# Optimization experiments

Measured on AMD Instinct MI355X. Metric: run time of the kernel, lower is better.

## Reference

```python
import jax, jax.numpy as jnp
import numpy as np

N_VERTS, N_RADIAL, N_ANGULAR, FEAT = 100000, 5, 8, 16
AMT_TEMPLATES, OUTPUT_DIM = 8, 32


def setup_inputs() -> dict:
    key = jax.random.key(0)
    k1, k2, k3, k4, k5, k6 = jax.random.split(key, 6)
    mesh_signal = jax.random.normal(k1, (N_VERTS, FEAT), dtype=jnp.float32)
    bary_weights = jax.random.uniform(k2, (N_VERTS, N_RADIAL, N_ANGULAR, 3), dtype=jnp.float32)
    interp_coeffs = jax.random.uniform(
        k3, (N_RADIAL, N_ANGULAR, N_RADIAL * N_ANGULAR), dtype=jnp.float32)
    template_weights = jax.random.normal(
        k4, (AMT_TEMPLATES, OUTPUT_DIM, FEAT), dtype=jnp.float32)
    bias = jax.random.normal(k5, (AMT_TEMPLATES, OUTPUT_DIM), dtype=jnp.float32)
    bary_indices = jax.random.randint(k6, (N_VERTS, N_RADIAL, N_ANGULAR, 3), 0, N_VERTS, dtype=jnp.int32)
    return {
        "mesh_signal": mesh_signal,
        "bary_weights": bary_weights,
        "interp_coeffs": interp_coeffs,
        "template_weights": template_weights,
        "bias": bias,
        "bary_indices": bary_indices,
    }


def reference(mesh_signal, bary_weights, interp_coeffs, template_weights, bias, bary_indices):
    n, R, A, _ = bary_indices.shape
    K = R * A
    # --- patch operator: barycentric gather + weighted interpolation ---
    gathered = mesh_signal[bary_indices]                         # (n, R, A, 3, F)
    interp = jnp.einsum('nrak,nrakf->nraf', bary_weights, gathered)  # (n, R, A, F)
    # --- prior: matvec with interpolation coefficients over flattened template ---
    flat = interp.reshape(n, K, -1)                              # (n, K, F)
    interp = jnp.einsum('nkf,rak->nraf', flat, interp_coeffs)    # (n, R, A, F)
    # --- fold: W @ X then reduce_sum over template-vertex axis. Since the
    # activation comes AFTER the reduce_sum, sum(W @ X, -1) == W @ sum(X, -1),
    # so we reduce first to avoid an (n, T, O, K) intermediate. ---
    s = interp.reshape(n, K, -1).sum(axis=1)                     # (n, F)
    pre = jnp.einsum('tof,nf->nto', template_weights, s) + bias  # (n, T, O)
    act = jax.nn.relu(pre)
    return act.sum(axis=1)                                       # (n, O)
```

## Files before the change

kernel.cpp:

```cpp
#include <hip/hip_runtime.h>

#define KK 40
#define M3 120
#define MM4 30
#define RCH 15
#define FEAT 16
#define NT 8
#define ODIM 32
#define VPB 32
#define BLOCK 256
#define SST 17

typedef unsigned int u32;
typedef unsigned short u16;
typedef float  f32x2 __attribute__((ext_vector_type(2)));
typedef float  f32x4 __attribute__((ext_vector_type(4)));
typedef int    i32x4 __attribute__((ext_vector_type(4)));
typedef u32    u32x4 __attribute__((ext_vector_type(4)));

__device__ __forceinline__ u16 f2bf_rne(float x) {
    u32 u = __float_as_uint(x);
    u32 r = (u + 0x7fffu + ((u >> 16) & 1u)) >> 16;
    return (u16)r;
}

__global__ void prep_kernel(const float* __restrict__ mesh, const float* __restrict__ ic,
                            u16* __restrict__ mbf, float* __restrict__ cs3, int total) {
    const int t = threadIdx.x;
    if (blockIdx.x == 0) {
        __shared__ float cs[KK];
        if (t < KK) {
            float s = 0.f;
            #pragma unroll
            for (int ra = 0; ra < KK; ++ra) s += ic[ra * KK + t];
            cs[t] = s;
        }
        __syncthreads();
        if (t < M3) cs3[t] = cs[t / 3];
        return;
    }
    const int i = (blockIdx.x - 1) * BLOCK + t;
    const int base = i * 8;
    if (base < total) {
        f32x4 a = __builtin_nontemporal_load((const f32x4*)(mesh + base));
        f32x4 b = __builtin_nontemporal_load((const f32x4*)(mesh + base + 4));
        u32x4 v;
        v.x = (u32)f2bf_rne(a.x) | ((u32)f2bf_rne(a.y) << 16);
        v.y = (u32)f2bf_rne(a.z) | ((u32)f2bf_rne(a.w) << 16);
        v.z = (u32)f2bf_rne(b.x) | ((u32)f2bf_rne(b.y) << 16);
        v.w = (u32)f2bf_rne(b.z) | ((u32)f2bf_rne(b.w) << 16);
        *(u32x4*)(mbf + base) = v;
    }
}

__device__ __forceinline__ void acc8(f32x2 acc2[4], const u32x4 g, const float s) {
    const f32x2 s2 = {s, s};
    f32x2 p;
    p.x = __uint_as_float(g.x << 16);
    p.y = __uint_as_float(g.x & 0xffff0000u);
    acc2[0] = __builtin_elementwise_fma(p, s2, acc2[0]);
    p.x = __uint_as_float(g.y << 16);
    p.y = __uint_as_float(g.y & 0xffff0000u);
    acc2[1] = __builtin_elementwise_fma(p, s2, acc2[1]);
    p.x = __uint_as_float(g.z << 16);
    p.y = __uint_as_float(g.z & 0xffff0000u);
    acc2[2] = __builtin_elementwise_fma(p, s2, acc2[2]);
    p.x = __uint_as_float(g.w << 16);
    p.y = __uint_as_float(g.w & 0xffff0000u);
    acc2[3] = __builtin_elementwise_fma(p, s2, acc2[3]);
}

__device__ __forceinline__ void issue4_sc0(const u32x4* p0, const u32x4* p1,
                                           const u32x4* p2, const u32x4* p3,
                                           u32x4& g0, u32x4& g1, u32x4& g2, u32x4& g3) {
    asm volatile(
        "global_load_dwordx4 %0, %4, off sc0\n\t"
        "global_load_dwordx4 %1, %5, off sc0\n\t"
        "global_load_dwordx4 %2, %6, off sc0\n\t"
        "global_load_dwordx4 %3, %7, off sc0"
        : "=&v"(g0), "=&v"(g1), "=&v"(g2), "=&v"(g3)
        : "v"(p0), "v"(p1), "v"(p2), "v"(p3)
        : "memory");
}

#define WAIT_VM4() do { asm volatile("s_waitcnt vmcnt(4)" ::: "memory"); \
                        __builtin_amdgcn_sched_barrier(0); } while (0)
#define WAIT_VM0() do { asm volatile("s_waitcnt vmcnt(0)" ::: "memory"); \
                        __builtin_amdgcn_sched_barrier(0); } while (0)

struct GBatch { u32x4 g0, g1, g2, g3; float w0, w1, w2, w3; };

__device__ __forceinline__ void prep_issue(GBatch& B,
                                           const f32x4* __restrict__ s_bw4,
                                           const i32x4* __restrict__ s_bi4,
                                           int row, int cbase, int jc, int q, int mc, int b,
                                           const u16* __restrict__ mbf) {
    const int s0 = 2 * b, s1 = 2 * b + 1;
    const bool v0 = (mc == 0) || (s0 < 7);
    const bool v1 = (mc == 0) || (s1 < 7);
    const f32x4 wq0 = s_bw4[row + cbase + (v0 ? s0 : 0)];
    const i32x4 iq0 = s_bi4[row + cbase + (v0 ? s0 : 0)];
    const f32x4 wq1 = s_bw4[row + cbase + (v1 ? s1 : 0)];
    const i32x4 iq1 = s_bi4[row + cbase + (v1 ? s1 : 0)];
    B.w0 = v0 ? (jc ? wq0.z : wq0.x) : 0.f;
    B.w1 = v0 ? (jc ? wq0.w : wq0.y) : 0.f;
    B.w2 = v1 ? (jc ? wq1.z : wq1.x) : 0.f;
    B.w3 = v1 ? (jc ? wq1.w : wq1.y) : 0.f;
    const int i0 = v0 ? (jc ? iq0.z : iq0.x) : 0;
    const int i1 = v0 ? (jc ? iq0.w : iq0.y) : 0;
    const int i2 = v1 ? (jc ? iq1.z : iq1.x) : 0;
    const int i3 = v1 ? (jc ? iq1.w : iq1.y) : 0;
    issue4_sc0((const u32x4*)(mbf + (size_t)i0 * FEAT) + q,
               (const u32x4*)(mbf + (size_t)i1 * FEAT) + q,
               (const u32x4*)(mbf + (size_t)i2 * FEAT) + q,
               (const u32x4*)(mbf + (size_t)i3 * FEAT) + q,
               B.g0, B.g1, B.g2, B.g3);
}

__device__ __forceinline__ void consume(f32x2 acc2[4], const GBatch& B) {
    acc8(acc2, B.g0, B.w0);
    acc8(acc2, B.g1, B.w1);
    acc8(acc2, B.g2, B.w2);
    acc8(acc2, B.g3, B.w3);
}

__global__ __launch_bounds__(BLOCK, 6) void conv_kernel(
    const u16*   __restrict__ mbf,
    const float* __restrict__ bw,
    const float* __restrict__ W,
    const float* __restrict__ bias,
    const int*   __restrict__ bi,
    const float* __restrict__ cs3,
    float*       __restrict__ out,
    int n)
{
    __shared__ f32x4 s_buf[VPB * SST * 2];
    __shared__ float s_sig[VPB][FEAT + 1];

    f32x4* s_bw4 = s_buf;
    i32x4* s_bi4 = (i32x4*)(s_buf + VPB * SST);
    float (*s_out)[ODIM + 1] = (float(*)[ODIM + 1])s_buf;

    const int tid = threadIdx.x;
    const int vg0 = blockIdx.x * VPB;

    const f32x4* bw4g  = (const f32x4*)bw;
    const i32x4* bi4g  = (const i32x4*)bi;
    const f32x4* cs34g = (const f32x4*)cs3;

    const int vloc = tid >> 3;
    const int jc   = (tid >> 2) & 1;
    const int mc   = (tid >> 1) & 1;
    const int q    = tid & 1;
    const int vg   = vg0 + vloc;

    f32x2 acc2[4];
    #pragma unroll
    for (int e = 0; e < 4; ++e) acc2[e] = (f32x2){0.f, 0.f};

    #pragma unroll
    for (int r = 0; r < 2; ++r) {
        if (r) __syncthreads();

        #pragma unroll
        for (int ii = 0; ii < 2; ++ii) {
            const int i = tid + ii * BLOCK;
            if (i < VPB * RCH) {
                const int v = i / RCH;
                const int c = i - v * RCH;
                if (vg0 + v < n) {
                    const int gchunk = (vg0 + v) * MM4 + r * RCH + c;
                    f32x4 wv = __builtin_nontemporal_load(bw4g + gchunk);
                    i32x4 iv = __builtin_nontemporal_load(bi4g + gchunk);
                    const f32x4 cc = cs34g[r * RCH + c];
                    wv.x *= cc.x; wv.y *= cc.y; wv.z *= cc.z; wv.w *= cc.w;
                    s_bw4[v * SST + c] = wv;
                    s_bi4[v * SST + c] = iv;
                }
            }
        }
        __syncthreads();

        if (vg < n) {
            const int row   = vloc * SST;
            const int cbase = mc ? 8 : 0;
            GBatch A, B, C, D;
            prep_issue(A, s_bw4, s_bi4, row, cbase, jc, q, mc, 0, mbf);
            prep_issue(B, s_bw4, s_bi4, row, cbase, jc, q, mc, 1, mbf);
            WAIT_VM4();
            consume(acc2, A);
            prep_issue(C, s_bw4, s_bi4, row, cbase, jc, q, mc, 2, mbf);
            WAIT_VM4();
            consume(acc2, B);
            prep_issue(D, s_bw4, s_bi4, row, cbase, jc, q, mc, 3, mbf);
            WAIT_VM4();
            consume(acc2, C);
            WAIT_VM0();
            consume(acc2, D);
        }
    }

    float a8[8] = { acc2[0].x, acc2[0].y, acc2[1].x, acc2[1].y,
                    acc2[2].x, acc2[2].y, acc2[3].x, acc2[3].y };
    #pragma unroll
    for (int e = 0; e < 8; ++e) a8[e] += __shfl_xor(a8[e], 4);
    #pragma unroll
    for (int e = 0; e < 8; ++e) a8[e] += __shfl_xor(a8[e], 2);

    if (jc == 0) {
        const f32x4 v = (mc == 0) ? (f32x4){a8[0], a8[1], a8[2], a8[3]}
                                  : (f32x4){a8[4], a8[5], a8[6], a8[7]};
        *(f32x4*)(&s_sig[vloc][q * 8 + mc * 4]) = v;
    }
    __syncthreads();

    {
        const int lane = tid & 63;
        const int wave = __builtin_amdgcn_readfirstlane(tid >> 6);
        const int v    = lane & (VPB - 1);

        float s[FEAT];
        #pragma unroll
        for (int f = 0; f < FEAT; ++f) s[f] = s_sig[v][f];

        float oacc[8];
        #pragma unroll
        for (int oi = 0; oi < 8; ++oi) oacc[oi] = 0.f;

        #pragma unroll 2
        for (int t = 0; t < NT; ++t) {
            #pragma unroll
            for (int oi = 0; oi < 8; ++oi) {
                const int o = wave * 8 + oi;
                float pre = bias[t * ODIM + o];
                const float* wrow = W + ((size_t)t * ODIM + o) * FEAT;
                #pragma unroll
                for (int f = 0; f < FEAT; ++f)
                    pre = fmaf(wrow[f], s[f], pre);
                oacc[oi] += fmaxf(pre, 0.f);
            }
        }

        if (lane < VPB) {
            #pragma unroll
            for (int oi = 0; oi < 8; ++oi)
                s_out[v][wave * 8 + oi] = oacc[oi];
        }
    }
    __syncthreads();

    {
        const int v   = tid >> 3;
        const int oq  = tid & 7;
        const int vgo = vg0 + v;
        if (vgo < n) {
            const f32x4 val = { s_out[v][oq * 4 + 0], s_out[v][oq * 4 + 1],
                                s_out[v][oq * 4 + 2], s_out[v][oq * 4 + 3] };
            *(f32x4*)(out + (size_t)vgo * ODIM + oq * 4) = val;
        }
    }
}

extern "C" void kernel_launch(void* const* d_in, const int* in_sizes, int n_in,
                              void* d_out, int out_size, void* d_ws, size_t ws_size,
                              hipStream_t stream) {
    const float* mesh = (const float*)d_in[0];
    const float* bw   = (const float*)d_in[1];
    const float* ic   = (const float*)d_in[2];
    const float* W    = (const float*)d_in[3];
    const float* bias = (const float*)d_in[4];
    const int*   bi   = (const int*)d_in[5];
    float* out = (float*)d_out;

    const int n = in_sizes[0] / FEAT;
    const int total = n * FEAT;

    float* cs3 = (float*)d_ws;
    u16*   mbf = (u16*)((char*)d_ws + 512);

    const int cvt_blocks = (total / 8 + BLOCK - 1) / BLOCK;
    prep_kernel<<<cvt_blocks + 1, BLOCK, 0, stream>>>(mesh, ic, mbf, cs3, total);

    const int blocks = (n + VPB - 1) / VPB;
    conv_kernel<<<blocks, BLOCK, 0, stream>>>(mbf, bw, W, bias, bi, cs3, out, n);
}
```

Before: 86.57 us.

## Double vertices per block and use packed fp32 FMA in template epilogue

Raises vertices per block from 32 to 64 and block size from 256 to 512. Each lane of the 8 waves now handles one distinct vertex and 4 outputs, instead of half the lanes duplicating 32 vertices over 8 outputs. The inner matvec uses two-wide vector FMA/max so the compiler can emit packed fp32 instructions. This removes the redundant duplicated epilogue work, but larger blocks may reduce occupancy and change the gather-phase mapping through the macros.

```diff
diff --git a/kernel.cpp b/kernel.cpp
--- a/kernel.cpp
+++ b/kernel.cpp
@@ -7,8 +7,8 @@
 #define FEAT 16
 #define NT 8
 #define ODIM 32
-#define VPB 32
-#define BLOCK 256
+#define VPB 64
+#define BLOCK 512
 #define SST 17
 
 typedef unsigned int u32;
@@ -217,35 +217,36 @@
     {
         const int lane = tid & 63;
         const int wave = __builtin_amdgcn_readfirstlane(tid >> 6);
-        const int v    = lane & (VPB - 1);
 
         float s[FEAT];
         #pragma unroll
-        for (int f = 0; f < FEAT; ++f) s[f] = s_sig[v][f];
-
-        float oacc[8];
-        #pragma unroll
-        for (int oi = 0; oi < 8; ++oi) oacc[oi] = 0.f;
+        for (int f = 0; f < FEAT; ++f) s[f] = s_sig[lane][f];
+
+        f32x2 oacc[2];
+        oacc[0] = (f32x2){0.f, 0.f};
+        oacc[1] = (f32x2){0.f, 0.f};
+        const f32x2 zero2 = {0.f, 0.f};
 
         #pragma unroll 2
         for (int t = 0; t < NT; ++t) {
             #pragma unroll
-            for (int oi = 0; oi < 8; ++oi) {
-                const int o = wave * 8 + oi;
-                float pre = bias[t * ODIM + o];
-                const float* wrow = W + ((size_t)t * ODIM + o) * FEAT;
+            for (int op = 0; op < 2; ++op) {
+                const int o0 = wave * 4 + op * 2;
+                f32x2 pre = { bias[t * ODIM + o0], bias[t * ODIM + o0 + 1] };
+                const float* w0 = W + ((size_t)t * ODIM + o0) * FEAT;
+                const float* w1 = w0 + FEAT;
                 #pragma unroll
-                for (int f = 0; f < FEAT; ++f)
-                    pre = fmaf(wrow[f], s[f], pre);
-                oacc[oi] += fmaxf(pre, 0.f);
+                for (int f = 0; f < FEAT; ++f) {
+                    const f32x2 wp = { w0[f], w1[f] };
+                    const f32x2 sp = { s[f], s[f] };
+                    pre = __builtin_elementwise_fma(wp, sp, pre);
+                }
+                oacc[op] += __builtin_elementwise_max(pre, zero2);
             }
         }
 
-        if (lane < VPB) {
-            #pragma unroll
-            for (int oi = 0; oi < 8; ++oi)
-                s_out[v][wave * 8 + oi] = oacc[oi];
-        }
+        *(f32x4*)(&s_out[lane][wave * 4]) =
+            (f32x4){oacc[0].x, oacc[0].y, oacc[1].x, oacc[1].y};
     }
     __syncthreads();
 
```

Result: slower. 89.13 us (+3.0%).
